# Kernel optimization log

Measured on AMD Instinct MI355X. Metric: run time of the kernel, lower is better.

Reference implementation:

```python
import jax, jax.numpy as jnp
import numpy as np

N = 50000        # nodes
E = 800000       # edges
IN, H1, H2 = 512, 256, 128
NEG_SLOPE = 0.2


def setup_inputs() -> dict:
    key = jax.random.key(0)
    k = jax.random.split(key, 6)
    X = jax.random.normal(k[0], (N, IN), jnp.float32)
    edge_index = jax.random.randint(k[1], (2, E), 0, N, dtype=jnp.int64)
    # GCNConv params: linear weight (no bias in lin) + additive bias
    W1 = jax.random.normal(k[2], (IN, H1), jnp.float32) / np.sqrt(IN).astype(np.float32)
    b1 = jnp.zeros((H1,), jnp.float32)
    W2 = jax.random.normal(k[3], (H1, H2), jnp.float32) / np.sqrt(H1).astype(np.float32)
    b2 = jnp.zeros((H2,), jnp.float32)
    return {"X": X, "edge_index": edge_index, "W1": W1, "b1": b1, "W2": W2, "b2": b2}


def gcn_conv(x, edge_index, W, b):
    """PyG GCNConv: X' = D^{-1/2} (A + I) D^{-1/2} (X W) + b."""
    src, dst = edge_index[0], edge_index[1]
    # degree with self-loops (unit edge weights)
    deg = jnp.zeros((N,), x.dtype).at[dst].add(jnp.asarray(1.0, x.dtype)) + 1.0
    dinv = jax.lax.rsqrt(deg)
    h = x @ W                                   # dense transform first (in >= out)
    coef = dinv[src] * dinv[dst]                # [E]
    msgs = h[src] * coef[:, None]               # [E, out]
    agg = jax.ops.segment_sum(msgs, dst, num_segments=N)
    agg = agg + (dinv * dinv)[:, None] * h      # self-loop contribution
    return agg + b


def reference(X, edge_index, W1, b1, W2, b2):
    Z = jax.nn.leaky_relu(gcn_conv(X, edge_index, W1, b1), NEG_SLOPE)
    Z = jax.nn.leaky_relu(gcn_conv(Z, edge_index, W2, b2), NEG_SLOPE)
    return Z
```

## Files before the change

kernel.cpp:

```cpp
#include <hip/hip_runtime.h>

constexpr int N_NODES = 50000;
constexpr int N_EDGES = 800000;
constexpr int F_IN  = 512;
constexpr int F_H1  = 256;
constexpr int F_H2  = 128;

typedef short  short8  __attribute__((ext_vector_type(8)));
typedef float  f32x4   __attribute__((ext_vector_type(4)));
typedef unsigned short us4 __attribute__((ext_vector_type(4)));

__device__ __forceinline__ unsigned short bf16_rn(float f) {
  unsigned int u = __float_as_uint(f);
  return (unsigned short)((u + 0x7FFFu + ((u >> 16) & 1u)) >> 16);
}
__device__ __forceinline__ float bf16_tof(unsigned short h) {
  return __uint_as_float(((unsigned int)h) << 16);
}


__global__ __launch_bounds__(256) void k_count(const int* __restrict__ dst,
                                               int* __restrict__ cnt, int e) {
  int i = blockIdx.x * 256 + threadIdx.x;
  if (i < e) atomicAdd(&cnt[dst[i]], 1);
}

__global__ __launch_bounds__(1024) void k_scan(const int* __restrict__ cnt,
                                               int* __restrict__ rowstart,
                                               int* __restrict__ cursor,
                                               float* __restrict__ dinv, int n) {
  __shared__ int wsum[16];
  __shared__ int carry_s;
  const int t = threadIdx.x;
  const int wid = t >> 6, lane = t & 63;
  if (t == 0) { carry_s = 0; rowstart[0] = 0; }
  __syncthreads();
  for (int base = 0; base < n; base += 4096) {
    const int i0 = base + t * 4;
    int v[4];
    if (i0 + 4 <= n) {
      const int4 v4 = *(const int4*)&cnt[i0];
      v[0] = v4.x; v[1] = v4.y; v[2] = v4.z; v[3] = v4.w;
    } else {
#pragma unroll
      for (int j = 0; j < 4; ++j) v[j] = (i0 + j < n) ? cnt[i0 + j] : 0;
    }
#pragma unroll
    for (int j = 0; j < 4; ++j)
      if (i0 + j < n) dinv[i0 + j] = rsqrtf((float)v[j] + 1.0f);
    const int tsum = v[0] + v[1] + v[2] + v[3];
    int x = tsum;
#pragma unroll
    for (int off = 1; off < 64; off <<= 1) {
      int y = __shfl_up(x, off);
      if (lane >= off) x += y;
    }
    if (lane == 63) wsum[wid] = x;
    __syncthreads();
    if (wid == 0) {
      int s = (lane < 16) ? wsum[lane] : 0;
#pragma unroll
      for (int off = 1; off < 16; off <<= 1) {
        int y = __shfl_up(s, off);
        if (lane >= off) s += y;
      }
      if (lane < 16) wsum[lane] = s;
    }
    __syncthreads();
    const int carry = carry_s;
    const int woff = (wid == 0) ? 0 : wsum[wid - 1];
    int run = carry + woff + x - tsum;
#pragma unroll
    for (int j = 0; j < 4; ++j) {
      if (i0 + j < n) {
        cursor[i0 + j] = run;
        run += v[j];
        rowstart[i0 + j + 1] = run;
      }
    }
    __syncthreads();
    if (t == 1023) carry_s = carry + woff + x;
    __syncthreads();
  }
}

__global__ __launch_bounds__(256) void k_fill(const int* __restrict__ src,
                                              const int* __restrict__ dst,
                                              int* __restrict__ cursor,
                                              const float* __restrict__ dinv,
                                              int2* __restrict__ csr, int e) {
  int i = blockIdx.x * 256 + threadIdx.x;
  if (i < e) {
    const int s = src[i], d = dst[i];
    int slot = atomicAdd(&cursor[d], 1);
    csr[slot] = make_int2(s, __float_as_int(dinv[s] * dinv[d]));
  }
}

__global__ __launch_bounds__(256) void k_wsplit2(const float* __restrict__ W1,
                                                 unsigned short* __restrict__ W1h,
                                                 unsigned short* __restrict__ W1l,
                                                 const float* __restrict__ W2,
                                                 unsigned short* __restrict__ W2h,
                                                 unsigned short* __restrict__ W2l) {
  constexpr int T1 = F_IN * F_H1;
  constexpr int T2 = F_H1 * F_H2;
  int id = blockIdx.x * 256 + threadIdx.x;
  if (id < T1) {
    int n = id / F_IN, k = id - n * F_IN;
    float f = W1[(size_t)k * F_H1 + n];
    unsigned short h = bf16_rn(f);
    W1h[id] = h;
    W1l[id] = bf16_rn(f - bf16_tof(h));
  } else if (id < T1 + T2) {
    int id2 = id - T1;
    int n = id2 / F_H1, k = id2 - n * F_H1;
    float f = W2[(size_t)k * F_H2 + n];
    unsigned short h = bf16_rn(f);
    W2h[id2] = h;
    W2l[id2] = bf16_rn(f - bf16_tof(h));
  }
}

template <bool A_IS_F32>
__global__ __launch_bounds__(512, 2) void k_mm(const float* __restrict__ Af,
                                               const unsigned short* __restrict__ Ah,
                                               const unsigned short* __restrict__ Bth,
                                               const unsigned short* __restrict__ Btl,
                                               unsigned short* __restrict__ Chh,
                                               unsigned short* __restrict__ Cll,
                                               int M, int N, int K) {
  __shared__ unsigned short Ah_s[128 * 64];
  __shared__ unsigned short Bh_s[128 * 64];
  __shared__ unsigned short Bl_s[128 * 64];
  const int tid = threadIdx.x;
  const int wid = tid >> 6, lane = tid & 63;
  const int wm = wid >> 2, wn = wid & 3;
  const int lr = lane & 15, lg = lane >> 4;
  const int col0 = blockIdx.x * 128, row0 = blockIdx.y * 128;

  f32x4 acc[4][2] = {};

  float4 af0[2], af1[2];
  short8 ahr[2];
  short8 bhr[2], blr[2];

  const int r_base = tid >> 3, g_ld = tid & 7;

  auto load_tile = [&](int k0) {
#pragma unroll
    for (int c = 0; c < 2; ++c) {
      const int r = c * 64 + r_base;
      const int gr = row0 + r;
      if (A_IS_F32) {
        af0[c] = make_float4(0.f, 0.f, 0.f, 0.f);
        af1[c] = af0[c];
        if (gr < M) {
          const float* ap = Af + (size_t)gr * K + k0 + g_ld * 8;
          af0[c] = *(const float4*)ap;
          af1[c] = *(const float4*)(ap + 4);
        }
      } else {
        ahr[c] = short8{};
        if (gr < M)
          ahr[c] = *(const short8*)&Ah[(size_t)gr * K + k0 + g_ld * 8];
      }
      const int gcol = col0 + r;
      bhr[c] = *(const short8*)&Bth[(size_t)gcol * K + k0 + g_ld * 8];
      blr[c] = *(const short8*)&Btl[(size_t)gcol * K + k0 + g_ld * 8];
    }
  };

  auto store_tile = [&]() {
#pragma unroll
    for (int c = 0; c < 2; ++c) {
      const int r = c * 64 + r_base;
      const int gs = g_ld ^ (r & 7);
      const int doff = r * 64 + gs * 8;
      if (A_IS_F32) {
        const float fv[8] = {af0[c].x, af0[c].y, af0[c].z, af0[c].w,
                             af1[c].x, af1[c].y, af1[c].z, af1[c].w};
        short8 hv;
#pragma unroll
        for (int j = 0; j < 8; ++j) hv[j] = (short)bf16_rn(fv[j]);
        *(short8*)&Ah_s[doff] = hv;
      } else {
        *(short8*)&Ah_s[doff] = ahr[c];
      }
      *(short8*)&Bh_s[doff] = bhr[c];
      *(short8*)&Bl_s[doff] = blr[c];
    }
  };

  const int nsteps = K >> 6;
  load_tile(0);
  for (int s = 0; s < nsteps; ++s) {
    store_tile();
    __syncthreads();
    if (s + 1 < nsteps) load_tile((s + 1) << 6);
#pragma unroll
    for (int kk = 0; kk < 2; ++kk) {
      short8 ah[4], bh[2], bl[2];
#pragma unroll
      for (int m = 0; m < 4; ++m) {
        const int r = wm * 64 + m * 16 + lr;
        const int g = kk * 4 + lg;
        ah[m] = *(const short8*)&Ah_s[r * 64 + (g ^ (r & 7)) * 8];
      }
#pragma unroll
      for (int n = 0; n < 2; ++n) {
        const int r = wn * 32 + n * 16 + lr;
        const int g = kk * 4 + lg;
        const int off = r * 64 + (g ^ (r & 7)) * 8;
        bh[n] = *(const short8*)&Bh_s[off];
        bl[n] = *(const short8*)&Bl_s[off];
      }
#pragma unroll
      for (int m = 0; m < 4; ++m)
#pragma unroll
        for (int n = 0; n < 2; ++n)
          acc[m][n] = __builtin_amdgcn_mfma_f32_16x16x32_bf16(ah[m], bh[n],
                                                              acc[m][n], 0, 0, 0);
#pragma unroll
      for (int m = 0; m < 4; ++m)
#pragma unroll
        for (int n = 0; n < 2; ++n)
          acc[m][n] = __builtin_amdgcn_mfma_f32_16x16x32_bf16(ah[m], bl[n],
                                                              acc[m][n], 0, 0, 0);
    }
    __syncthreads();
  }
#pragma unroll
  for (int m = 0; m < 4; ++m) {
#pragma unroll
    for (int j = 0; j < 4; ++j) {
      const int row = row0 + wm * 64 + m * 16 + (lane >> 4) * 4 + j;
      if (row < M) {
        const size_t base = (size_t)row * N + col0 + wn * 32 + lr;
#pragma unroll
        for (int n = 0; n < 2; ++n) {
          const float v = acc[m][n][j];
          const unsigned short hv = bf16_rn(v);
          Chh[base + n * 16] = hv;
          Cll[base + n * 16] = bf16_rn(v - bf16_tof(hv));
        }
      }
    }
  }
}

template <int F, bool SPLIT_OUT>
__global__ __launch_bounds__(256) void k_agg(const unsigned short* __restrict__ hh,
                                             const unsigned short* __restrict__ hl,
                                             const int* __restrict__ rowstart,
                                             const int2* __restrict__ csr,
                                             const float* __restrict__ dinv,
                                             const float* __restrict__ bias,
                                             float* __restrict__ outp,
                                             unsigned short* __restrict__ outh,
                                             int n) {
  constexpr int V = F / 64;
  const int node = (blockIdx.x * 256 + threadIdx.x) >> 6;
  const int lane = threadIdx.x & 63;
  if (node >= n) return;
  const float dn = dinv[node];
  const int e0 = rowstart[node];
  const int cnt = rowstart[node + 1] - e0;
  const int2* cp = csr + e0;
  float acc[V] = {};
  int i = 0;

  auto gather = [&](int s, float f[V]) {
    if constexpr (V == 4) {
      const uint2 u = *(const uint2*)(hh + (size_t)s * F + lane * 4);
      f[0] = __uint_as_float(u.x << 16);
      f[1] = __uint_as_float(u.x & 0xffff0000u);
      f[2] = __uint_as_float(u.y << 16);
      f[3] = __uint_as_float(u.y & 0xffff0000u);
    } else {
      const unsigned int u = *(const unsigned int*)(hh + (size_t)s * F + lane * 2);
      f[0] = __uint_as_float(u << 16);
      f[1] = __uint_as_float(u & 0xffff0000u);
    }
  };

  for (; i + 4 <= cnt; i += 4) {
    const int2 p0 = cp[i], p1 = cp[i + 1], p2 = cp[i + 2], p3 = cp[i + 3];
    float f0[V], f1[V], f2[V], f3[V];
    gather(p0.x, f0);
    gather(p1.x, f1);
    gather(p2.x, f2);
    gather(p3.x, f3);
    const float c0 = __int_as_float(p0.y), c1 = __int_as_float(p1.y);
    const float c2 = __int_as_float(p2.y), c3 = __int_as_float(p3.y);
#pragma unroll
    for (int j = 0; j < V; ++j)
      acc[j] += c0 * f0[j] + c1 * f1[j] + c2 * f2[j] + c3 * f3[j];
  }
  for (; i < cnt; ++i) {
    const int2 p = cp[i];
    const float c = __int_as_float(p.y);
    float f[V];
    gather(p.x, f);
#pragma unroll
    for (int j = 0; j < V; ++j) acc[j] += c * f[j];
  }

  const float sc = dn * dn;
  const unsigned short* shp = hh + (size_t)node * F + lane * V;
  const unsigned short* slp = hl + (size_t)node * F + lane * V;
  const float* bp = bias + lane * V;
  float r[V];
#pragma unroll
  for (int j = 0; j < V; ++j) {
    const float hself = bf16_tof(shp[j]) + bf16_tof(slp[j]);
    float t = acc[j] + sc * hself + bp[j];
    r[j] = fmaxf(t, 0.2f * t);
  }
  if constexpr (SPLIT_OUT) {
    unsigned short hv[V];
#pragma unroll
    for (int j = 0; j < V; ++j) hv[j] = bf16_rn(r[j]);
    if constexpr (V == 4) {
      *(us4*)&outh[(size_t)node * F + lane * 4] = us4{hv[0], hv[1], hv[2], hv[3]};
    } else {
#pragma unroll
      for (int j = 0; j < V; ++j) outh[(size_t)node * F + lane * V + j] = hv[j];
    }
  } else {
    float* op = outp + (size_t)node * F + lane * V;
    if constexpr (V == 4) {
      *(float4*)op = make_float4(r[0], r[1], r[2], r[3]);
    } else {
      *(float2*)op = make_float2(r[0], r[1]);
    }
  }
}

extern "C" void kernel_launch(void* const* d_in, const int* in_sizes, int n_in,
                              void* d_out, int out_size, void* d_ws, size_t ws_size,
                              hipStream_t stream) {
  const float* X  = (const float*)d_in[0];
  const int*   ei = (const int*)d_in[1];
  const float* W1 = (const float*)d_in[2];
  const float* b1 = (const float*)d_in[3];
  const float* W2 = (const float*)d_in[4];
  const float* b2 = (const float*)d_in[5];
  float* out = (float*)d_out;
  const int* src = ei;
  const int* dst = ei + N_EDGES;

  char* p = (char*)d_ws;
  unsigned short* h1h = (unsigned short*)p; p += (size_t)N_NODES * F_H1 * 2;
  unsigned short* h1l = (unsigned short*)p; p += (size_t)N_NODES * F_H1 * 2;
  unsigned short* z1h = (unsigned short*)p; p += (size_t)N_NODES * F_H1 * 2;
  unsigned short* Wt1h = (unsigned short*)p; p += (size_t)F_IN * F_H1 * 2;
  unsigned short* Wt1l = (unsigned short*)p; p += (size_t)F_IN * F_H1 * 2;
  unsigned short* Wt2h = (unsigned short*)p; p += (size_t)F_H1 * F_H2 * 2;
  unsigned short* Wt2l = (unsigned short*)p; p += (size_t)F_H1 * F_H2 * 2;
  float* dinv = (float*)p;                  p += 50048 * 4;
  int* counts = (int*)p;                    p += 50048 * 4;
  int* rowstart = (int*)p;                  p += 50056 * 4;
  int* cursor = (int*)p;                    p += 50048 * 4;
  int2* csr = (int2*)p;                     p += (size_t)N_EDGES * 8;
  unsigned short* h2h = h1h;
  unsigned short* h2l = h1l;

  hipMemsetAsync(counts, 0, N_NODES * sizeof(int), stream);
  k_count<<<(N_EDGES + 255) / 256, 256, 0, stream>>>(dst, counts, N_EDGES);
  k_scan<<<1, 1024, 0, stream>>>(counts, rowstart, cursor, dinv, N_NODES);
  k_fill<<<(N_EDGES + 255) / 256, 256, 0, stream>>>(src, dst, cursor, dinv, csr,
                                                    N_EDGES);

  k_wsplit2<<<(F_IN * F_H1 + F_H1 * F_H2 + 255) / 256, 256, 0, stream>>>(
      W1, Wt1h, Wt1l, W2, Wt2h, Wt2l);

  dim3 g1(F_H1 / 128, (N_NODES + 127) / 128);
  k_mm<true><<<g1, 512, 0, stream>>>(X, nullptr, Wt1h, Wt1l, h1h, h1l,
                                     N_NODES, F_H1, F_IN);
  k_agg<F_H1, true><<<(N_NODES + 3) / 4, 256, 0, stream>>>(
      h1h, h1l, rowstart, csr, dinv, b1, nullptr, z1h, N_NODES);

  dim3 g2(F_H2 / 128, (N_NODES + 127) / 128);
  k_mm<false><<<g2, 512, 0, stream>>>(nullptr, z1h, Wt2h, Wt2l, h2h, h2l,
                                      N_NODES, F_H2, F_H1);
  k_agg<F_H2, false><<<(N_NODES + 3) / 4, 256, 0, stream>>>(
      h2h, h2l, rowstart, csr, dinv, b2, out, nullptr, N_NODES);
}
```

Before: 303.7 us.

## Fuse layer-1 aggregation with layer-2 matmul and merge prep kernels

The layer-1 neighbor aggregation now writes each block's 16 node rows of z1 into swizzled shared memory. The same block then multiplies them by W2 with bf16 MFMA, which removes the z1 global round-trip and one kernel launch. The edge-degree count is also folded into the weight-split kernel, saving another launch. The tradeoff is that each wave aggregates 4 nodes serially before a block barrier, and W2 is re-read from global or L2 by every block.

```diff
diff --git a/kernel.cpp b/kernel.cpp
--- a/kernel.cpp
+++ b/kernel.cpp
@@ -18,11 +18,34 @@
   return __uint_as_float(((unsigned int)h) << 16);
 }
 
-
-__global__ __launch_bounds__(256) void k_count(const int* __restrict__ dst,
-                                               int* __restrict__ cnt, int e) {
-  int i = blockIdx.x * 256 + threadIdx.x;
-  if (i < e) atomicAdd(&cnt[dst[i]], 1);
+__global__ __launch_bounds__(256) void k_prep(const float* __restrict__ W1,
+                                              unsigned short* __restrict__ W1h,
+                                              unsigned short* __restrict__ W1l,
+                                              const float* __restrict__ W2,
+                                              unsigned short* __restrict__ W2h,
+                                              unsigned short* __restrict__ W2l,
+                                              const int* __restrict__ dst,
+                                              int* __restrict__ cnt) {
+  constexpr int T1 = F_IN * F_H1;
+  constexpr int T2 = F_H1 * F_H2;
+  constexpr int TW = T1 + T2;
+  int id = blockIdx.x * 256 + threadIdx.x;
+  if (id < T1) {
+    int n = id / F_IN, k = id - n * F_IN;
+    float f = W1[(size_t)k * F_H1 + n];
+    unsigned short h = bf16_rn(f);
+    W1h[id] = h;
+    W1l[id] = bf16_rn(f - bf16_tof(h));
+  } else if (id < TW) {
+    int id2 = id - T1;
+    int n = id2 / F_H1, k = id2 - n * F_H1;
+    float f = W2[(size_t)k * F_H2 + n];
+    unsigned short h = bf16_rn(f);
+    W2h[id2] = h;
+    W2l[id2] = bf16_rn(f - bf16_tof(h));
+  } else if (id - TW < N_EDGES) {
+    atomicAdd(&cnt[dst[id - TW]], 1);
+  }
 }
 
 __global__ __launch_bounds__(1024) void k_scan(const int* __restrict__ cnt,
@@ -97,31 +120,6 @@
   }
 }
 
-__global__ __launch_bounds__(256) void k_wsplit2(const float* __restrict__ W1,
-                                                 unsigned short* __restrict__ W1h,
-                                                 unsigned short* __restrict__ W1l,
-                                                 const float* __restrict__ W2,
-                                                 unsigned short* __restrict__ W2h,
-                                                 unsigned short* __restrict__ W2l) {
-  constexpr int T1 = F_IN * F_H1;
-  constexpr int T2 = F_H1 * F_H2;
-  int id = blockIdx.x * 256 + threadIdx.x;
-  if (id < T1) {
-    int n = id / F_IN, k = id - n * F_IN;
-    float f = W1[(size_t)k * F_H1 + n];
-    unsigned short h = bf16_rn(f);
-    W1h[id] = h;
-    W1l[id] = bf16_rn(f - bf16_tof(h));
-  } else if (id < T1 + T2) {
-    int id2 = id - T1;
-    int n = id2 / F_H1, k = id2 - n * F_H1;
-    float f = W2[(size_t)k * F_H2 + n];
-    unsigned short h = bf16_rn(f);
-    W2h[id2] = h;
-    W2l[id2] = bf16_rn(f - bf16_tof(h));
-  }
-}
-
 template <bool A_IS_F32>
 __global__ __launch_bounds__(512, 2) void k_mm(const float* __restrict__ Af,
                                                const unsigned short* __restrict__ Ah,
@@ -249,17 +247,111 @@
   }
 }
 
-template <int F, bool SPLIT_OUT>
-__global__ __launch_bounds__(256) void k_agg(const unsigned short* __restrict__ hh,
-                                             const unsigned short* __restrict__ hl,
-                                             const int* __restrict__ rowstart,
-                                             const int2* __restrict__ csr,
-                                             const float* __restrict__ dinv,
-                                             const float* __restrict__ bias,
-                                             float* __restrict__ outp,
-                                             unsigned short* __restrict__ outh,
-                                             int n) {
-  constexpr int V = F / 64;
+__global__ __launch_bounds__(256) void k_aggmm(
+    const unsigned short* __restrict__ hh, const unsigned short* __restrict__ hl,
+    const int* __restrict__ rowstart, const int2* __restrict__ csr,
+    const float* __restrict__ dinv, const float* __restrict__ bias,
+    const unsigned short* __restrict__ W2h, const unsigned short* __restrict__ W2l,
+    unsigned short* __restrict__ h2h, unsigned short* __restrict__ h2l, int n) {
+  __shared__ unsigned short z1s[16 * 256];
+  const int tid = threadIdx.x;
+  const int w = tid >> 6, lane = tid & 63;
+  const int nb = blockIdx.x * 16;
+
+  for (int i = 0; i < 4; ++i) {
+    const int node = nb + w * 4 + i;
+    const float dn = dinv[node];
+    const int e0 = rowstart[node];
+    const int cnt = rowstart[node + 1] - e0;
+    const int2* cp = csr + e0;
+    float a0 = 0.f, a1 = 0.f, a2 = 0.f, a3 = 0.f;
+    int e = 0;
+    for (; e + 4 <= cnt; e += 4) {
+      const int2 p0 = cp[e], p1 = cp[e + 1], p2 = cp[e + 2], p3 = cp[e + 3];
+      const uint2 u0 = *(const uint2*)(hh + (size_t)p0.x * F_H1 + lane * 4);
+      const uint2 u1 = *(const uint2*)(hh + (size_t)p1.x * F_H1 + lane * 4);
+      const uint2 u2 = *(const uint2*)(hh + (size_t)p2.x * F_H1 + lane * 4);
+      const uint2 u3 = *(const uint2*)(hh + (size_t)p3.x * F_H1 + lane * 4);
+      const float c0 = __int_as_float(p0.y), c1 = __int_as_float(p1.y);
+      const float c2 = __int_as_float(p2.y), c3 = __int_as_float(p3.y);
+      a0 += c0 * __uint_as_float(u0.x << 16) + c1 * __uint_as_float(u1.x << 16) +
+            c2 * __uint_as_float(u2.x << 16) + c3 * __uint_as_float(u3.x << 16);
+      a1 += c0 * __uint_as_float(u0.x & 0xffff0000u) +
+            c1 * __uint_as_float(u1.x & 0xffff0000u) +
+            c2 * __uint_as_float(u2.x & 0xffff0000u) +
+            c3 * __uint_as_float(u3.x & 0xffff0000u);
+      a2 += c0 * __uint_as_float(u0.y << 16) + c1 * __uint_as_float(u1.y << 16) +
+            c2 * __uint_as_float(u2.y << 16) + c3 * __uint_as_float(u3.y << 16);
+      a3 += c0 * __uint_as_float(u0.y & 0xffff0000u) +
+            c1 * __uint_as_float(u1.y & 0xffff0000u) +
+            c2 * __uint_as_float(u2.y & 0xffff0000u) +
+            c3 * __uint_as_float(u3.y & 0xffff0000u);
+    }
+    for (; e < cnt; ++e) {
+      const int2 pp = cp[e];
+      const float c = __int_as_float(pp.y);
+      const uint2 u = *(const uint2*)(hh + (size_t)pp.x * F_H1 + lane * 4);
+      a0 += c * __uint_as_float(u.x << 16);
+      a1 += c * __uint_as_float(u.x & 0xffff0000u);
+      a2 += c * __uint_as_float(u.y << 16);
+      a3 += c * __uint_as_float(u.y & 0xffff0000u);
+    }
+    const float sc = dn * dn;
+    const unsigned short* shp = hh + (size_t)node * F_H1 + lane * 4;
+    const unsigned short* slp = hl + (size_t)node * F_H1 + lane * 4;
+    const float* bp = bias + lane * 4;
+    float r[4] = {a0, a1, a2, a3};
+#pragma unroll
+    for (int j = 0; j < 4; ++j) {
+      const float hself = bf16_tof(shp[j]) + bf16_tof(slp[j]);
+      float t = r[j] + sc * hself + bp[j];
+      r[j] = fmaxf(t, 0.2f * t);
+    }
+    const int row = w * 4 + i;
+    const int gi = (lane >> 1) ^ (row & 7);
+    unsigned short* dp = &z1s[row * 256 + gi * 8 + (lane & 1) * 4];
+    *(us4*)dp = us4{bf16_rn(r[0]), bf16_rn(r[1]), bf16_rn(r[2]), bf16_rn(r[3])};
+  }
+  __syncthreads();
+
+  const int lr = lane & 15, lg = lane >> 4;
+  f32x4 acc[2] = {{0.f, 0.f, 0.f, 0.f}, {0.f, 0.f, 0.f, 0.f}};
+  const int col0 = w * 32;
+#pragma unroll
+  for (int kk = 0; kk < 8; ++kk) {
+    const int gi = kk * 4 + lg;
+    const short8 a = *(const short8*)&z1s[lr * 256 + (gi ^ (lr & 7)) * 8];
+#pragma unroll
+    for (int nn = 0; nn < 2; ++nn) {
+      const int col = col0 + nn * 16 + lr;
+      const short8 bh = *(const short8*)&W2h[(size_t)col * F_H1 + kk * 32 + lg * 8];
+      const short8 bl = *(const short8*)&W2l[(size_t)col * F_H1 + kk * 32 + lg * 8];
+      acc[nn] = __builtin_amdgcn_mfma_f32_16x16x32_bf16(a, bh, acc[nn], 0, 0, 0);
+      acc[nn] = __builtin_amdgcn_mfma_f32_16x16x32_bf16(a, bl, acc[nn], 0, 0, 0);
+    }
+  }
+#pragma unroll
+  for (int nn = 0; nn < 2; ++nn) {
+#pragma unroll
+    for (int j = 0; j < 4; ++j) {
+      const int node = nb + (lane >> 4) * 4 + j;
+      const int col = col0 + nn * 16 + (lane & 15);
+      const float v = acc[nn][j];
+      const unsigned short hv = bf16_rn(v);
+      h2h[(size_t)node * F_H2 + col] = hv;
+      h2l[(size_t)node * F_H2 + col] = bf16_rn(v - bf16_tof(hv));
+    }
+  }
+}
+
+__global__ __launch_bounds__(256) void k_agg2(const unsigned short* __restrict__ hh,
+                                              const unsigned short* __restrict__ hl,
+                                              const int* __restrict__ rowstart,
+                                              const int2* __restrict__ csr,
+                                              const float* __restrict__ dinv,
+                                              const float* __restrict__ bias,
+                                              float* __restrict__ outp, int n) {
+  constexpr int F = F_H2;
   const int node = (blockIdx.x * 256 + threadIdx.x) >> 6;
   const int lane = threadIdx.x & 63;
   if (node >= n) return;
@@ -267,74 +359,41 @@
   const int e0 = rowstart[node];
   const int cnt = rowstart[node + 1] - e0;
   const int2* cp = csr + e0;
-  float acc[V] = {};
+  float a0 = 0.f, a1 = 0.f;
   int i = 0;
-
-  auto gather = [&](int s, float f[V]) {
-    if constexpr (V == 4) {
-      const uint2 u = *(const uint2*)(hh + (size_t)s * F + lane * 4);
-      f[0] = __uint_as_float(u.x << 16);
-      f[1] = __uint_as_float(u.x & 0xffff0000u);
-      f[2] = __uint_as_float(u.y << 16);
-      f[3] = __uint_as_float(u.y & 0xffff0000u);
-    } else {
-      const unsigned int u = *(const unsigned int*)(hh + (size_t)s * F + lane * 2);
-      f[0] = __uint_as_float(u << 16);
-      f[1] = __uint_as_float(u & 0xffff0000u);
-    }
-  };
-
   for (; i + 4 <= cnt; i += 4) {
     const int2 p0 = cp[i], p1 = cp[i + 1], p2 = cp[i + 2], p3 = cp[i + 3];
-    float f0[V], f1[V], f2[V], f3[V];
-    gather(p0.x, f0);
-    gather(p1.x, f1);
-    gather(p2.x, f2);
-    gather(p3.x, f3);
+    const unsigned int u0 = *(const unsigned int*)(hh + (size_t)p0.x * F + lane * 2);
+    const unsigned int u1 = *(const unsigned int*)(hh + (size_t)p1.x * F + lane * 2);
+    const unsigned int u2 = *(const unsigned int*)(hh + (size_t)p2.x * F + lane * 2);
+    const unsigned int u3 = *(const unsigned int*)(hh + (size_t)p3.x * F + lane * 2);
     const float c0 = __int_as_float(p0.y), c1 = __int_as_float(p1.y);
     const float c2 = __int_as_float(p2.y), c3 = __int_as_float(p3.y);
-#pragma unroll
-    for (int j = 0; j < V; ++j)
-      acc[j] += c0 * f0[j] + c1 * f1[j] + c2 * f2[j] + c3 * f3[j];
+    a0 += c0 * __uint_as_float(u0 << 16) + c1 * __uint_as_float(u1 << 16) +
+          c2 * __uint_as_float(u2 << 16) + c3 * __uint_as_float(u3 << 16);
+    a1 += c0 * __uint_as_float(u0 & 0xffff0000u) +
+          c1 * __uint_as_float(u1 & 0xffff0000u) +
+          c2 * __uint_as_float(u2 & 0xffff0000u) +
+          c3 * __uint_as_float(u3 & 0xffff0000u);
   }
   for (; i < cnt; ++i) {
-    const int2 p = cp[i];
-    const float c = __int_as_float(p.y);
-    float f[V];
-    gather(p.x, f);
-#pragma unroll
-    for (int j = 0; j < V; ++j) acc[j] += c * f[j];
-  }
-
+    const int2 pp = cp[i];
+    const float c = __int_as_float(pp.y);
+    const unsigned int u = *(const unsigned int*)(hh + (size_t)pp.x * F + lane * 2);
+    a0 += c * __uint_as_float(u << 16);
+    a1 += c * __uint_as_float(u & 0xffff0000u);
+  }
   const float sc = dn * dn;
-  const unsigned short* shp = hh + (size_t)node * F + lane * V;
-  const unsigned short* slp = hl + (size_t)node * F + lane * V;
-  const float* bp = bias + lane * V;
-  float r[V];
-#pragma unroll
-  for (int j = 0; j < V; ++j) {
-    const float hself = bf16_tof(shp[j]) + bf16_tof(slp[j]);
-    float t = acc[j] + sc * hself + bp[j];
-    r[j] = fmaxf(t, 0.2f * t);
-  }
-  if constexpr (SPLIT_OUT) {
-    unsigned short hv[V];
-#pragma unroll
-    for (int j = 0; j < V; ++j) hv[j] = bf16_rn(r[j]);
-    if constexpr (V == 4) {
-      *(us4*)&outh[(size_t)node * F + lane * 4] = us4{hv[0], hv[1], hv[2], hv[3]};
-    } else {
-#pragma unroll
-      for (int j = 0; j < V; ++j) outh[(size_t)node * F + lane * V + j] = hv[j];
-    }
-  } else {
-    float* op = outp + (size_t)node * F + lane * V;
-    if constexpr (V == 4) {
-      *(float4*)op = make_float4(r[0], r[1], r[2], r[3]);
-    } else {
-      *(float2*)op = make_float2(r[0], r[1]);
-    }
-  }
+  const unsigned short* shp = hh + (size_t)node * F + lane * 2;
+  const unsigned short* slp = hl + (size_t)node * F + lane * 2;
+  const float* bp = bias + lane * 2;
+  const float h0 = bf16_tof(shp[0]) + bf16_tof(slp[0]);
+  const float h1v = bf16_tof(shp[1]) + bf16_tof(slp[1]);
+  float t0 = a0 + sc * h0 + bp[0];
+  float t1 = a1 + sc * h1v + bp[1];
+  t0 = fmaxf(t0, 0.2f * t0);
+  t1 = fmaxf(t1, 0.2f * t1);
+  *(float2*)(outp + (size_t)node * F + lane * 2) = make_float2(t0, t1);
 }
 
 extern "C" void kernel_launch(void* const* d_in, const int* in_sizes, int n_in,
@@ -353,7 +412,8 @@
   char* p = (char*)d_ws;
   unsigned short* h1h = (unsigned short*)p; p += (size_t)N_NODES * F_H1 * 2;
   unsigned short* h1l = (unsigned short*)p; p += (size_t)N_NODES * F_H1 * 2;
-  unsigned short* z1h = (unsigned short*)p; p += (size_t)N_NODES * F_H1 * 2;
+  unsigned short* h2h = (unsigned short*)p; p += (size_t)N_NODES * F_H2 * 2;
+  unsigned short* h2l = (unsigned short*)p; p += (size_t)N_NODES * F_H2 * 2;
   unsigned short* Wt1h = (unsigned short*)p; p += (size_t)F_IN * F_H1 * 2;
   unsigned short* Wt1l = (unsigned short*)p; p += (size_t)F_IN * F_H1 * 2;
   unsigned short* Wt2h = (unsigned short*)p; p += (size_t)F_H1 * F_H2 * 2;
@@ -363,27 +423,22 @@
   int* rowstart = (int*)p;                  p += 50056 * 4;
   int* cursor = (int*)p;                    p += 50048 * 4;
   int2* csr = (int2*)p;                     p += (size_t)N_EDGES * 8;
-  unsigned short* h2h = h1h;
-  unsigned short* h2l = h1l;
 
   hipMemsetAsync(counts, 0, N_NODES * sizeof(int), stream);
-  k_count<<<(N_EDGES + 255) / 256, 256, 0, stream>>>(dst, counts, N_EDGES);
+  constexpr int PREP_IDS = F_IN * F_H1 + F_H1 * F_H2 + N_EDGES;
+  k_prep<<<(PREP_IDS + 255) / 256, 256, 0, stream>>>(W1, Wt1h, Wt1l, W2, Wt2h,
+                                                     Wt2l, dst, counts);
   k_scan<<<1, 1024, 0, stream>>>(counts, rowstart, cursor, dinv, N_NODES);
   k_fill<<<(N_EDGES + 255) / 256, 256, 0, stream>>>(src, dst, cursor, dinv, csr,
                                                     N_EDGES);
 
-  k_wsplit2<<<(F_IN * F_H1 + F_H1 * F_H2 + 255) / 256, 256, 0, stream>>>(
-      W1, Wt1h, Wt1l, W2, Wt2h, Wt2l);
-
   dim3 g1(F_H1 / 128, (N_NODES + 127) / 128);
   k_mm<true><<<g1, 512, 0, stream>>>(X, nullptr, Wt1h, Wt1l, h1h, h1l,
                                      N_NODES, F_H1, F_IN);
-  k_agg<F_H1, true><<<(N_NODES + 3) / 4, 256, 0, stream>>>(
-      h1h, h1l, rowstart, csr, dinv, b1, nullptr, z1h, N_NODES);
-
-  dim3 g2(F_H2 / 128, (N_NODES + 127) / 128);
-  k_mm<false><<<g2, 512, 0, stream>>>(nullptr, z1h, Wt2h, Wt2l, h2h, h2l,
-                                      N_NODES, F_H2, F_H1);
-  k_agg<F_H2, false><<<(N_NODES + 3) / 4, 256, 0, stream>>>(
-      h2h, h2l, rowstart, csr, dinv, b2, out, nullptr, N_NODES);
-}
+
+  k_aggmm<<<N_NODES / 16, 256, 0, stream>>>(h1h, h1l, rowstart, csr, dinv, b1,
+                                            Wt2h, Wt2l, h2h, h2l, N_NODES);
+
+  k_agg2<<<(N_NODES + 3) / 4, 256, 0, stream>>>(h2h, h2l, rowstart, csr, dinv,
+                                                b2, out, N_NODES);
+}
```

Result: slower. 329.4 us (+8.4%).

## Shrink GEMM K-tile to 32 and fuse weight split with degree count

Applied to the files above, without the earlier changes.

The GEMM kernel now uses a K tile of 32 instead of 64. That cuts shared memory from 48KB to 24KB per block and changes the loading so each thread moves one 8-element chunk per tile, with a new XOR swizzle. Separately, the weight bf16 hi/lo split and the edge degree-count atomics are merged into one kernel launch, removing a launch. The smaller tile doubles the number of barrier-synchronised steps and halves the MFMA work per sync, which may expose more latency in exchange for lower LDS pressure and possibly higher occupancy.

```diff
diff --git a/kernel.cpp b/kernel.cpp
--- a/kernel.cpp
+++ b/kernel.cpp
@@ -18,11 +18,34 @@
   return __uint_as_float(((unsigned int)h) << 16);
 }
 
-
-__global__ __launch_bounds__(256) void k_count(const int* __restrict__ dst,
-                                               int* __restrict__ cnt, int e) {
-  int i = blockIdx.x * 256 + threadIdx.x;
-  if (i < e) atomicAdd(&cnt[dst[i]], 1);
+__global__ __launch_bounds__(256) void k_prep(const float* __restrict__ W1,
+                                              unsigned short* __restrict__ W1h,
+                                              unsigned short* __restrict__ W1l,
+                                              const float* __restrict__ W2,
+                                              unsigned short* __restrict__ W2h,
+                                              unsigned short* __restrict__ W2l,
+                                              const int* __restrict__ dst,
+                                              int* __restrict__ cnt) {
+  constexpr int T1 = F_IN * F_H1;
+  constexpr int T2 = F_H1 * F_H2;
+  constexpr int TW = T1 + T2;
+  int id = blockIdx.x * 256 + threadIdx.x;
+  if (id < T1) {
+    int n = id / F_IN, k = id - n * F_IN;
+    float f = W1[(size_t)k * F_H1 + n];
+    unsigned short h = bf16_rn(f);
+    W1h[id] = h;
+    W1l[id] = bf16_rn(f - bf16_tof(h));
+  } else if (id < TW) {
+    int id2 = id - T1;
+    int n = id2 / F_H1, k = id2 - n * F_H1;
+    float f = W2[(size_t)k * F_H2 + n];
+    unsigned short h = bf16_rn(f);
+    W2h[id2] = h;
+    W2l[id2] = bf16_rn(f - bf16_tof(h));
+  } else if (id - TW < N_EDGES) {
+    atomicAdd(&cnt[dst[id - TW]], 1);
+  }
 }
 
 __global__ __launch_bounds__(1024) void k_scan(const int* __restrict__ cnt,
@@ -97,31 +120,6 @@
   }
 }
 
-__global__ __launch_bounds__(256) void k_wsplit2(const float* __restrict__ W1,
-                                                 unsigned short* __restrict__ W1h,
-                                                 unsigned short* __restrict__ W1l,
-                                                 const float* __restrict__ W2,
-                                                 unsigned short* __restrict__ W2h,
-                                                 unsigned short* __restrict__ W2l) {
-  constexpr int T1 = F_IN * F_H1;
-  constexpr int T2 = F_H1 * F_H2;
-  int id = blockIdx.x * 256 + threadIdx.x;
-  if (id < T1) {
-    int n = id / F_IN, k = id - n * F_IN;
-    float f = W1[(size_t)k * F_H1 + n];
-    unsigned short h = bf16_rn(f);
-    W1h[id] = h;
-    W1l[id] = bf16_rn(f - bf16_tof(h));
-  } else if (id < T1 + T2) {
-    int id2 = id - T1;
-    int n = id2 / F_H1, k = id2 - n * F_H1;
-    float f = W2[(size_t)k * F_H2 + n];
-    unsigned short h = bf16_rn(f);
-    W2h[id2] = h;
-    W2l[id2] = bf16_rn(f - bf16_tof(h));
-  }
-}
-
 template <bool A_IS_F32>
 __global__ __launch_bounds__(512, 2) void k_mm(const float* __restrict__ Af,
                                                const unsigned short* __restrict__ Ah,
@@ -130,9 +128,9 @@
                                                unsigned short* __restrict__ Chh,
                                                unsigned short* __restrict__ Cll,
                                                int M, int N, int K) {
-  __shared__ unsigned short Ah_s[128 * 64];
-  __shared__ unsigned short Bh_s[128 * 64];
-  __shared__ unsigned short Bl_s[128 * 64];
+  __shared__ unsigned short Ah_s[128 * 32];
+  __shared__ unsigned short Bh_s[128 * 32];
+  __shared__ unsigned short Bl_s[128 * 32];
   const int tid = threadIdx.x;
   const int wid = tid >> 6, lane = tid & 63;
   const int wm = wid >> 2, wn = wid & 3;
@@ -141,93 +139,78 @@
 
   f32x4 acc[4][2] = {};
 
-  float4 af0[2], af1[2];
-  short8 ahr[2];
-  short8 bhr[2], blr[2];
-
-  const int r_base = tid >> 3, g_ld = tid & 7;
+  const int r_s = tid >> 2, g_s = tid & 3;
+  const int doff = r_s * 32 + (g_s ^ ((r_s >> 1) & 3)) * 8;
+  const bool a_ok = (row0 + r_s) < M;
+  const size_t a_row = (size_t)(row0 + r_s) * K;
+  const size_t b_row = (size_t)(col0 + r_s) * K;
+
+  float4 af0, af1;
+  short8 ahr, bhr, blr;
 
   auto load_tile = [&](int k0) {
-#pragma unroll
-    for (int c = 0; c < 2; ++c) {
-      const int r = c * 64 + r_base;
-      const int gr = row0 + r;
-      if (A_IS_F32) {
-        af0[c] = make_float4(0.f, 0.f, 0.f, 0.f);
-        af1[c] = af0[c];
-        if (gr < M) {
-          const float* ap = Af + (size_t)gr * K + k0 + g_ld * 8;
-          af0[c] = *(const float4*)ap;
-          af1[c] = *(const float4*)(ap + 4);
-        }
-      } else {
-        ahr[c] = short8{};
-        if (gr < M)
-          ahr[c] = *(const short8*)&Ah[(size_t)gr * K + k0 + g_ld * 8];
+    const int kk = k0 + g_s * 8;
+    if (A_IS_F32) {
+      af0 = make_float4(0.f, 0.f, 0.f, 0.f);
+      af1 = af0;
+      if (a_ok) {
+        const float* ap = Af + a_row + kk;
+        af0 = *(const float4*)ap;
+        af1 = *(const float4*)(ap + 4);
       }
-      const int gcol = col0 + r;
-      bhr[c] = *(const short8*)&Bth[(size_t)gcol * K + k0 + g_ld * 8];
-      blr[c] = *(const short8*)&Btl[(size_t)gcol * K + k0 + g_ld * 8];
-    }
+    } else {
+      ahr = short8{};
+      if (a_ok) ahr = *(const short8*)&Ah[a_row + kk];
+    }
+    bhr = *(const short8*)&Bth[b_row + kk];
+    blr = *(const short8*)&Btl[b_row + kk];
   };
 
   auto store_tile = [&]() {
-#pragma unroll
-    for (int c = 0; c < 2; ++c) {
-      const int r = c * 64 + r_base;
-      const int gs = g_ld ^ (r & 7);
-      const int doff = r * 64 + gs * 8;
-      if (A_IS_F32) {
-        const float fv[8] = {af0[c].x, af0[c].y, af0[c].z, af0[c].w,
-                             af1[c].x, af1[c].y, af1[c].z, af1[c].w};
-        short8 hv;
-#pragma unroll
-        for (int j = 0; j < 8; ++j) hv[j] = (short)bf16_rn(fv[j]);
-        *(short8*)&Ah_s[doff] = hv;
-      } else {
-        *(short8*)&Ah_s[doff] = ahr[c];
-      }
-      *(short8*)&Bh_s[doff] = bhr[c];
-      *(short8*)&Bl_s[doff] = blr[c];
-    }
+    if (A_IS_F32) {
+      const float fv[8] = {af0.x, af0.y, af0.z, af0.w, af1.x, af1.y, af1.z, af1.w};
+      short8 hv;
+#pragma unroll
+      for (int j = 0; j < 8; ++j) hv[j] = (short)bf16_rn(fv[j]);
+      *(short8*)&Ah_s[doff] = hv;
+    } else {
+      *(short8*)&Ah_s[doff] = ahr;
+    }
+    *(short8*)&Bh_s[doff] = bhr;
+    *(short8*)&Bl_s[doff] = blr;
   };
 
-  const int nsteps = K >> 6;
+  const int nsteps = K >> 5;
   load_tile(0);
   for (int s = 0; s < nsteps; ++s) {
     store_tile();
     __syncthreads();
-    if (s + 1 < nsteps) load_tile((s + 1) << 6);
-#pragma unroll
-    for (int kk = 0; kk < 2; ++kk) {
-      short8 ah[4], bh[2], bl[2];
-#pragma unroll
-      for (int m = 0; m < 4; ++m) {
-        const int r = wm * 64 + m * 16 + lr;
-        const int g = kk * 4 + lg;
-        ah[m] = *(const short8*)&Ah_s[r * 64 + (g ^ (r & 7)) * 8];
-      }
-#pragma unroll
-      for (int n = 0; n < 2; ++n) {
-        const int r = wn * 32 + n * 16 + lr;
-        const int g = kk * 4 + lg;
-        const int off = r * 64 + (g ^ (r & 7)) * 8;
-        bh[n] = *(const short8*)&Bh_s[off];
-        bl[n] = *(const short8*)&Bl_s[off];
-      }
-#pragma unroll
-      for (int m = 0; m < 4; ++m)
-#pragma unroll
-        for (int n = 0; n < 2; ++n)
-          acc[m][n] = __builtin_amdgcn_mfma_f32_16x16x32_bf16(ah[m], bh[n],
-                                                              acc[m][n], 0, 0, 0);
-#pragma unroll
-      for (int m = 0; m < 4; ++m)
-#pragma unroll
-        for (int n = 0; n < 2; ++n)
-          acc[m][n] = __builtin_amdgcn_mfma_f32_16x16x32_bf16(ah[m], bl[n],
-                                                              acc[m][n], 0, 0, 0);
-    }
+    if (s + 1 < nsteps) load_tile((s + 1) << 5);
+    short8 ah[4], bh[2], bl[2];
+#pragma unroll
+    for (int m = 0; m < 4; ++m) {
+      const int r = wm * 64 + m * 16 + lr;
+      ah[m] = *(const short8*)&Ah_s[r * 32 + (lg ^ ((r >> 1) & 3)) * 8];
+    }
+#pragma unroll
+    for (int n = 0; n < 2; ++n) {
+      const int r = wn * 32 + n * 16 + lr;
+      const int off = r * 32 + (lg ^ ((r >> 1) & 3)) * 8;
+      bh[n] = *(const short8*)&Bh_s[off];
+      bl[n] = *(const short8*)&Bl_s[off];
+    }
+#pragma unroll
+    for (int m = 0; m < 4; ++m)
+#pragma unroll
+      for (int n = 0; n < 2; ++n)
+        acc[m][n] = __builtin_amdgcn_mfma_f32_16x16x32_bf16(ah[m], bh[n],
+                                                            acc[m][n], 0, 0, 0);
+#pragma unroll
+    for (int m = 0; m < 4; ++m)
+#pragma unroll
+      for (int n = 0; n < 2; ++n)
+        acc[m][n] = __builtin_amdgcn_mfma_f32_16x16x32_bf16(ah[m], bl[n],
+                                                            acc[m][n], 0, 0, 0);
     __syncthreads();
   }
 #pragma unroll
@@ -367,13 +350,12 @@
   unsigned short* h2l = h1l;
 
   hipMemsetAsync(counts, 0, N_NODES * sizeof(int), stream);
-  k_count<<<(N_EDGES + 255) / 256, 256, 0, stream>>>(dst, counts, N_EDGES);
+  constexpr int PREP_IDS = F_IN * F_H1 + F_H1 * F_H2 + N_EDGES;
+  k_prep<<<(PREP_IDS + 255) / 256, 256, 0, stream>>>(W1, Wt1h, Wt1l, W2, Wt2h,
+                                                     Wt2l, dst, counts);
   k_scan<<<1, 1024, 0, stream>>>(counts, rowstart, cursor, dinv, N_NODES);
   k_fill<<<(N_EDGES + 255) / 256, 256, 0, stream>>>(src, dst, cursor, dinv, csr,
                                                     N_EDGES);
-
-  k_wsplit2<<<(F_IN * F_H1 + F_H1 * F_H2 + 255) / 256, 256, 0, stream>>>(
-      W1, Wt1h, Wt1l, W2, Wt2h, Wt2l);
 
   dim3 g1(F_H1 / 128, (N_NODES + 127) / 128);
   k_mm<true><<<g1, 512, 0, stream>>>(X, nullptr, Wt1h, Wt1l, h1h, h1l,
```

Result: no change. 300.9 us (-0.9%).

## Slice aggregation by feature columns and fuse degree count into weight prep

Applied to the files above, without the earlier changes.

The aggregation kernel now splits each node's feature row into 32-column slices, one per block. Each 16-lane group handles one node, so a 64-lane wave covers four nodes and adjacent blocks cover adjacent slices, aiming for better cache locality on the gathered rows. CSR entries are read with nontemporal loads. The degree-count atomics are merged into the weight-split kernel to save a launch. The trade-off is that each node's CSR list is reread once per slice, and the gathers become narrower 4-byte loads per lane.

```diff
diff --git a/kernel.cpp b/kernel.cpp
--- a/kernel.cpp
+++ b/kernel.cpp
@@ -17,12 +17,41 @@
 __device__ __forceinline__ float bf16_tof(unsigned short h) {
   return __uint_as_float(((unsigned int)h) << 16);
 }
-
-
-__global__ __launch_bounds__(256) void k_count(const int* __restrict__ dst,
-                                               int* __restrict__ cnt, int e) {
-  int i = blockIdx.x * 256 + threadIdx.x;
-  if (i < e) atomicAdd(&cnt[dst[i]], 1);
+__device__ __forceinline__ float bf_lo(unsigned int u) {
+  return __uint_as_float(u << 16);
+}
+__device__ __forceinline__ float bf_hi(unsigned int u) {
+  return __uint_as_float(u & 0xffff0000u);
+}
+
+__global__ __launch_bounds__(256) void k_prep(const float* __restrict__ W1,
+                                              unsigned short* __restrict__ W1h,
+                                              unsigned short* __restrict__ W1l,
+                                              const float* __restrict__ W2,
+                                              unsigned short* __restrict__ W2h,
+                                              unsigned short* __restrict__ W2l,
+                                              const int* __restrict__ dst,
+                                              int* __restrict__ cnt) {
+  constexpr int T1 = F_IN * F_H1;
+  constexpr int T2 = F_H1 * F_H2;
+  constexpr int TW = T1 + T2;
+  int id = blockIdx.x * 256 + threadIdx.x;
+  if (id < T1) {
+    int n = id / F_IN, k = id - n * F_IN;
+    float f = W1[(size_t)k * F_H1 + n];
+    unsigned short h = bf16_rn(f);
+    W1h[id] = h;
+    W1l[id] = bf16_rn(f - bf16_tof(h));
+  } else if (id < TW) {
+    int id2 = id - T1;
+    int n = id2 / F_H1, k = id2 - n * F_H1;
+    float f = W2[(size_t)k * F_H2 + n];
+    unsigned short h = bf16_rn(f);
+    W2h[id2] = h;
+    W2l[id2] = bf16_rn(f - bf16_tof(h));
+  } else if (id - TW < N_EDGES) {
+    atomicAdd(&cnt[dst[id - TW]], 1);
+  }
 }
 
 __global__ __launch_bounds__(1024) void k_scan(const int* __restrict__ cnt,
@@ -97,31 +126,6 @@
   }
 }
 
-__global__ __launch_bounds__(256) void k_wsplit2(const float* __restrict__ W1,
-                                                 unsigned short* __restrict__ W1h,
-                                                 unsigned short* __restrict__ W1l,
-                                                 const float* __restrict__ W2,
-                                                 unsigned short* __restrict__ W2h,
-                                                 unsigned short* __restrict__ W2l) {
-  constexpr int T1 = F_IN * F_H1;
-  constexpr int T2 = F_H1 * F_H2;
-  int id = blockIdx.x * 256 + threadIdx.x;
-  if (id < T1) {
-    int n = id / F_IN, k = id - n * F_IN;
-    float f = W1[(size_t)k * F_H1 + n];
-    unsigned short h = bf16_rn(f);
-    W1h[id] = h;
-    W1l[id] = bf16_rn(f - bf16_tof(h));
-  } else if (id < T1 + T2) {
-    int id2 = id - T1;
-    int n = id2 / F_H1, k = id2 - n * F_H1;
-    float f = W2[(size_t)k * F_H2 + n];
-    unsigned short h = bf16_rn(f);
-    W2h[id2] = h;
-    W2l[id2] = bf16_rn(f - bf16_tof(h));
-  }
-}
-
 template <bool A_IS_F32>
 __global__ __launch_bounds__(512, 2) void k_mm(const float* __restrict__ Af,
                                                const unsigned short* __restrict__ Ah,
@@ -249,91 +253,63 @@
   }
 }
 
-template <int F, bool SPLIT_OUT>
-__global__ __launch_bounds__(256) void k_agg(const unsigned short* __restrict__ hh,
-                                             const unsigned short* __restrict__ hl,
-                                             const int* __restrict__ rowstart,
-                                             const int2* __restrict__ csr,
-                                             const float* __restrict__ dinv,
-                                             const float* __restrict__ bias,
-                                             float* __restrict__ outp,
-                                             unsigned short* __restrict__ outh,
-                                             int n) {
-  constexpr int V = F / 64;
-  const int node = (blockIdx.x * 256 + threadIdx.x) >> 6;
-  const int lane = threadIdx.x & 63;
+template <int F, int NSLICE, bool SPLIT_OUT>
+__global__ __launch_bounds__(256) void k_aggs(
+    const unsigned short* __restrict__ hh, const unsigned short* __restrict__ hl,
+    const int* __restrict__ rowstart, const int2* __restrict__ csr,
+    const float* __restrict__ dinv, const float* __restrict__ bias,
+    float* __restrict__ outp, unsigned short* __restrict__ outh, int n) {
+  const int bid = blockIdx.x;
+  const int slice = bid & (NSLICE - 1);
+  const int chunk = bid / NSLICE;
+  const int tid = threadIdx.x;
+  const int w = tid >> 6, lane = tid & 63;
+  const int g = lane >> 4, l16 = lane & 15;
+  const int node = chunk * 16 + w * 4 + g;
   if (node >= n) return;
+  const int colb = slice * 32 + l16 * 2;
   const float dn = dinv[node];
   const int e0 = rowstart[node];
   const int cnt = rowstart[node + 1] - e0;
   const int2* cp = csr + e0;
-  float acc[V] = {};
+  float a0 = 0.f, a1 = 0.f;
   int i = 0;
-
-  auto gather = [&](int s, float f[V]) {
-    if constexpr (V == 4) {
-      const uint2 u = *(const uint2*)(hh + (size_t)s * F + lane * 4);
-      f[0] = __uint_as_float(u.x << 16);
-      f[1] = __uint_as_float(u.x & 0xffff0000u);
-      f[2] = __uint_as_float(u.y << 16);
-      f[3] = __uint_as_float(u.y & 0xffff0000u);
-    } else {
-      const unsigned int u = *(const unsigned int*)(hh + (size_t)s * F + lane * 2);
-      f[0] = __uint_as_float(u << 16);
-      f[1] = __uint_as_float(u & 0xffff0000u);
-    }
-  };
-
   for (; i + 4 <= cnt; i += 4) {
-    const int2 p0 = cp[i], p1 = cp[i + 1], p2 = cp[i + 2], p3 = cp[i + 3];
-    float f0[V], f1[V], f2[V], f3[V];
-    gather(p0.x, f0);
-    gather(p1.x, f1);
-    gather(p2.x, f2);
-    gather(p3.x, f3);
-    const float c0 = __int_as_float(p0.y), c1 = __int_as_float(p1.y);
-    const float c2 = __int_as_float(p2.y), c3 = __int_as_float(p3.y);
-#pragma unroll
-    for (int j = 0; j < V; ++j)
-      acc[j] += c0 * f0[j] + c1 * f1[j] + c2 * f2[j] + c3 * f3[j];
+    const long long q0 = __builtin_nontemporal_load((const long long*)(cp + i));
+    const long long q1 = __builtin_nontemporal_load((const long long*)(cp + i + 1));
+    const long long q2 = __builtin_nontemporal_load((const long long*)(cp + i + 2));
+    const long long q3 = __builtin_nontemporal_load((const long long*)(cp + i + 3));
+    const unsigned int u0 = *(const unsigned int*)(hh + (size_t)(int)q0 * F + colb);
+    const unsigned int u1 = *(const unsigned int*)(hh + (size_t)(int)q1 * F + colb);
+    const unsigned int u2 = *(const unsigned int*)(hh + (size_t)(int)q2 * F + colb);
+    const unsigned int u3 = *(const unsigned int*)(hh + (size_t)(int)q3 * F + colb);
+    const float c0 = __int_as_float((int)(q0 >> 32));
+    const float c1 = __int_as_float((int)(q1 >> 32));
+    const float c2 = __int_as_float((int)(q2 >> 32));
+    const float c3 = __int_as_float((int)(q3 >> 32));
+    a0 += c0 * bf_lo(u0) + c1 * bf_lo(u1) + c2 * bf_lo(u2) + c3 * bf_lo(u3);
+    a1 += c0 * bf_hi(u0) + c1 * bf_hi(u1) + c2 * bf_hi(u2) + c3 * bf_hi(u3);
   }
   for (; i < cnt; ++i) {
-    const int2 p = cp[i];
-    const float c = __int_as_float(p.y);
-    float f[V];
-    gather(p.x, f);
-#pragma unroll
-    for (int j = 0; j < V; ++j) acc[j] += c * f[j];
-  }
-
+    const long long q = __builtin_nontemporal_load((const long long*)(cp + i));
+    const unsigned int u = *(const unsigned int*)(hh + (size_t)(int)q * F + colb);
+    const float c = __int_as_float((int)(q >> 32));
+    a0 += c * bf_lo(u);
+    a1 += c * bf_hi(u);
+  }
   const float sc = dn * dn;
-  const unsigned short* shp = hh + (size_t)node * F + lane * V;
-  const unsigned short* slp = hl + (size_t)node * F + lane * V;
-  const float* bp = bias + lane * V;
-  float r[V];
-#pragma unroll
-  for (int j = 0; j < V; ++j) {
-    const float hself = bf16_tof(shp[j]) + bf16_tof(slp[j]);
-    float t = acc[j] + sc * hself + bp[j];
-    r[j] = fmaxf(t, 0.2f * t);
-  }
+  const unsigned int sh = *(const unsigned int*)(hh + (size_t)node * F + colb);
+  const unsigned int sl = *(const unsigned int*)(hl + (size_t)node * F + colb);
+  float t0 = a0 + sc * (bf_lo(sh) + bf_lo(sl)) + bias[colb];
+  float t1 = a1 + sc * (bf_hi(sh) + bf_hi(sl)) + bias[colb + 1];
+  t0 = fmaxf(t0, 0.2f * t0);
+  t1 = fmaxf(t1, 0.2f * t1);
   if constexpr (SPLIT_OUT) {
-    unsigned short hv[V];
-#pragma unroll
-    for (int j = 0; j < V; ++j) hv[j] = bf16_rn(r[j]);
-    if constexpr (V == 4) {
-      *(us4*)&outh[(size_t)node * F + lane * 4] = us4{hv[0], hv[1], hv[2], hv[3]};
-    } else {
-#pragma unroll
-      for (int j = 0; j < V; ++j) outh[(size_t)node * F + lane * V + j] = hv[j];
-    }
+    const unsigned int pk =
+        (unsigned int)bf16_rn(t0) | ((unsigned int)bf16_rn(t1) << 16);
+    *(unsigned int*)&outh[(size_t)node * F + colb] = pk;
   } else {
-    float* op = outp + (size_t)node * F + lane * V;
-    if constexpr (V == 4) {
-      *(float4*)op = make_float4(r[0], r[1], r[2], r[3]);
-    } else {
-      *(float2*)op = make_float2(r[0], r[1]);
-    }
+    *(float2*)&outp[(size_t)node * F + colb] = make_float2(t0, t1);
   }
 }
 
@@ -367,23 +343,22 @@
   unsigned short* h2l = h1l;
 
   hipMemsetAsync(counts, 0, N_NODES * sizeof(int), stream);
-  k_count<<<(N_EDGES + 255) / 256, 256, 0, stream>>>(dst, counts, N_EDGES);
+  constexpr int PREP_IDS = F_IN * F_H1 + F_H1 * F_H2 + N_EDGES;
+  k_prep<<<(PREP_IDS + 255) / 256, 256, 0, stream>>>(W1, Wt1h, Wt1l, W2, Wt2h,
+                                                     Wt2l, dst, counts);
   k_scan<<<1, 1024, 0, stream>>>(counts, rowstart, cursor, dinv, N_NODES);
   k_fill<<<(N_EDGES + 255) / 256, 256, 0, stream>>>(src, dst, cursor, dinv, csr,
                                                     N_EDGES);
 
-  k_wsplit2<<<(F_IN * F_H1 + F_H1 * F_H2 + 255) / 256, 256, 0, stream>>>(
-      W1, Wt1h, Wt1l, W2, Wt2h, Wt2l);
-
   dim3 g1(F_H1 / 128, (N_NODES + 127) / 128);
   k_mm<true><<<g1, 512, 0, stream>>>(X, nullptr, Wt1h, Wt1l, h1h, h1l,
                                      N_NODES, F_H1, F_IN);
-  k_agg<F_H1, true><<<(N_NODES + 3) / 4, 256, 0, stream>>>(
+  k_aggs<F_H1, 8, true><<<8 * (N_NODES / 16), 256, 0, stream>>>(
       h1h, h1l, rowstart, csr, dinv, b1, nullptr, z1h, N_NODES);
 
   dim3 g2(F_H2 / 128, (N_NODES + 127) / 128);
   k_mm<false><<<g2, 512, 0, stream>>>(nullptr, z1h, Wt2h, Wt2l, h2h, h2l,
                                       N_NODES, F_H2, F_H1);
-  k_agg<F_H2, false><<<(N_NODES + 3) / 4, 256, 0, stream>>>(
+  k_aggs<F_H2, 4, false><<<4 * (N_NODES / 16), 256, 0, stream>>>(
       h2h, h2l, rowstart, csr, dinv, b2, out, nullptr, N_NODES);
 }
```

New measurement: 431.5 us. 42.1% more time.
